# Kernel tuning notes

Hardware: AMD Instinct MI355X
Metric: run time of the kernel (lower is better)

Reference implementation:

```python
import jax, jax.numpy as jnp
import numpy as np

EMB = 1024
HEADS = 16
HEAD_DIM = EMB // HEADS


def setup_inputs() -> dict:
    key = jax.random.key(0)
    ks = jax.random.split(key, 9)
    s = 1.0 / np.sqrt(EMB)
    x = jax.random.normal(ks[0], (4, 2048, EMB), dtype=jnp.float32)
    Wq = jax.random.uniform(ks[1], (EMB, EMB), minval=-s, maxval=s, dtype=jnp.float32)
    bq = jax.random.uniform(ks[2], (EMB,), minval=-s, maxval=s, dtype=jnp.float32)
    Wk = jax.random.uniform(ks[3], (EMB, EMB), minval=-s, maxval=s, dtype=jnp.float32)
    bk = jax.random.uniform(ks[4], (EMB,), minval=-s, maxval=s, dtype=jnp.float32)
    Wv = jax.random.uniform(ks[5], (EMB, EMB), minval=-s, maxval=s, dtype=jnp.float32)
    bv = jax.random.uniform(ks[6], (EMB,), minval=-s, maxval=s, dtype=jnp.float32)
    Wo = jax.random.uniform(ks[7], (EMB, EMB), minval=-s, maxval=s, dtype=jnp.float32)
    bo = jax.random.uniform(ks[8], (EMB,), minval=-s, maxval=s, dtype=jnp.float32)
    return {"x": x, "Wq": Wq, "bq": bq, "Wk": Wk, "bk": bk, "Wv": Wv, "bv": bv, "Wo": Wo, "bo": bo}


def reference(x, Wq, bq, Wk, bk, Wv, bv, Wo, bo):
    B, S, E = x.shape
    # QKV projections (torch Linear: y = x W^T + b)
    q = x @ Wq.T + bq
    k = x @ Wk.T + bk
    v = x @ Wv.T + bv
    # split heads -> [B, H, S, Dh]
    q = q.reshape(B, S, HEADS, HEAD_DIM).transpose(0, 2, 1, 3)
    k = k.reshape(B, S, HEADS, HEAD_DIM).transpose(0, 2, 1, 3)
    v = v.reshape(B, S, HEADS, HEAD_DIM).transpose(0, 2, 1, 3)
    # NOTE: module scales by 1/sqrt(emb_size), NOT 1/sqrt(head_dim)
    scale = 1.0 / jnp.sqrt(jnp.asarray(E, dtype=x.dtype))
    energy = jnp.einsum('bhqd,bhkd->bhqk', q, k) * scale
    attention = jax.nn.softmax(energy, axis=-1)
    out = jnp.einsum('bhqk,bhkd->bhqd', attention, v)
    out = out.transpose(0, 2, 1, 3).reshape(B, S, E)
    return out @ Wo.T + bo
```

## Files before the change

kernel.cpp:

```cpp
#include <hip/hip_runtime.h>


typedef __bf16 bf16;
typedef __attribute__((ext_vector_type(8))) short short8;
typedef __attribute__((ext_vector_type(4))) float floatx4;
typedef __attribute__((ext_vector_type(2))) unsigned int uintx2;
typedef __attribute__((ext_vector_type(4))) unsigned int uintx4;

#define MFMA16(a, b, c) __builtin_amdgcn_mfma_f32_16x16x32_bf16((a), (b), (c), 0, 0, 0)

#define LDS_STRIDE 56

__device__ __forceinline__ float fast_exp2(float x) {
    float r;
    asm("v_exp_f32 %0, %1" : "=v"(r) : "v"(x));
    return r;
}
__device__ __forceinline__ unsigned int cvt_pk_bf16(float lo, float hi) {
    unsigned int r;
    asm("v_cvt_pk_bf16_f32 %0, %1, %2" : "=v"(r) : "v"(lo), "v"(hi));
    return r;
}

__device__ __forceinline__ void async16(const bf16* __restrict__ g, short* l) {
    __builtin_amdgcn_global_load_lds((const __attribute__((address_space(1))) void*)g,
                                     (__attribute__((address_space(3))) void*)l, 16, 0, 0);
}

__device__ __forceinline__ short8 frag8(const bf16* __restrict__ p) {
    return *(const short8*)p;
}
__device__ __forceinline__ short8 frag8(const float* __restrict__ p) {
    const floatx4 a = *(const floatx4*)p;
    const floatx4 b = *(const floatx4*)(p + 4);
    short8 r;
#pragma unroll
    for (int j = 0; j < 4; j++) {
        r[j]     = __builtin_bit_cast(short, (bf16)a[j]);
        r[4 + j] = __builtin_bit_cast(short, (bf16)b[j]);
    }
    return r;
}

__global__ __launch_bounds__(256) void to_bf16(
    const float* __restrict__ in, bf16* __restrict__ out, int n8)
{
    const int i = blockIdx.x * 256 + threadIdx.x;
    if (i >= n8) return;
    const floatx4 a = *(const floatx4*)(in + (size_t)i * 8);
    const floatx4 b = *(const floatx4*)(in + (size_t)i * 8 + 4);
    short8 r;
#pragma unroll
    for (int j = 0; j < 4; j++) {
        r[j]     = __builtin_bit_cast(short, (bf16)a[j]);
        r[4 + j] = __builtin_bit_cast(short, (bf16)b[j]);
    }
    *(short8*)((short*)out + (size_t)i * 8) = r;
}

template <typename TB>
__device__ __forceinline__ void gemm128_async(
    const bf16* __restrict__ A, const TB* __restrict__ B,
    int m0, int n0, short* As, short* Bs, floatx4 acc[4][4])
{
    constexpr bool BASYNC = (sizeof(TB) == 2);
    const int tid  = threadIdx.x;
    const int lane = tid & 63;
    const int w    = tid >> 6;
    const int wu   = __builtin_amdgcn_readfirstlane(w);
    const int wm   = w >> 1, wn = w & 1;
    const int g    = lane >> 4, c = lane & 15;
    const int ar = lane >> 2;
    const int aq = ((lane & 3) ^ (ar & 3)) * 8;
    const int lrow = tid >> 2;
    const int lc8  = (tid & 3) * 8;

#pragma unroll
    for (int mi = 0; mi < 4; mi++)
#pragma unroll
        for (int ni = 0; ni < 4; ni++)
            acc[mi][ni] = (floatx4){0.f, 0.f, 0.f, 0.f};

    const int aswz = (g ^ (c & 3)) * 8;

    for (int k0 = 0; k0 < 1024; k0 += 32) {
        async16(A + (size_t)(m0 + w * 32 + ar) * 1024 + k0 + aq,      As + wu * 1024);
        async16(A + (size_t)(m0 + w * 32 + 16 + ar) * 1024 + k0 + aq, As + wu * 1024 + 512);
        if constexpr (BASYNC) {
            const bf16* Bb = (const bf16*)B;
            async16(Bb + (size_t)(n0 + w * 32 + ar) * 1024 + k0 + aq,      Bs + wu * 1024);
            async16(Bb + (size_t)(n0 + w * 32 + 16 + ar) * 1024 + k0 + aq, Bs + wu * 1024 + 512);
        } else {
            *(short8*)(Bs + lrow * LDS_STRIDE + lc8) =
                frag8(B + (size_t)(n0 + lrow) * 1024 + k0 + lc8);
            *(short8*)(Bs + (lrow + 64) * LDS_STRIDE + lc8) =
                frag8(B + (size_t)(n0 + lrow + 64) * 1024 + k0 + lc8);
        }
        __syncthreads();

        short8 af[4], bfr[4];
#pragma unroll
        for (int mi = 0; mi < 4; mi++)
            af[mi] = *(const short8*)(As + (wm * 64 + mi * 16 + c) * 32 + aswz);
#pragma unroll
        for (int ni = 0; ni < 4; ni++) {
            if constexpr (BASYNC)
                bfr[ni] = *(const short8*)(Bs + (wn * 64 + ni * 16 + c) * 32 + aswz);
            else
                bfr[ni] = *(const short8*)(Bs + (wn * 64 + ni * 16 + c) * LDS_STRIDE + g * 8);
        }
#pragma unroll
        for (int mi = 0; mi < 4; mi++)
#pragma unroll
            for (int ni = 0; ni < 4; ni++)
                acc[mi][ni] = MFMA16(af[mi], bfr[ni], acc[mi][ni]);
        __syncthreads();
    }
}

template <typename TB>
__global__ __launch_bounds__(256) void qkv_gemm(
    const bf16* __restrict__ Xb,
    const TB* __restrict__ Wq, const TB* __restrict__ Wk, const TB* __restrict__ Wv,
    const float* __restrict__ bq, const float* __restrict__ bk, const float* __restrict__ bv,
    bf16* __restrict__ qkv)
{
    __shared__ __align__(16) short As[128 * 32];
    __shared__ __align__(16) short Bs[(sizeof(TB) == 2) ? 128 * 32 : 128 * LDS_STRIDE];

    const int z = blockIdx.z;
    const TB* W       = (z == 0) ? Wq : (z == 1) ? Wk : Wv;
    const float* bias = (z == 0) ? bq : (z == 1) ? bk : bv;
    bf16* outz = qkv + (size_t)z * (8192u * 1024u);

    const int m0 = blockIdx.y * 128;
    const int n0 = blockIdx.x * 128;

    floatx4 acc[4][4];
    gemm128_async(Xb, W, m0, n0, As, Bs, acc);

    const int lane = threadIdx.x & 63;
    const int w = threadIdx.x >> 6;
    const int wm = w >> 1, wn = w & 1;
    const int g = lane >> 4, c = lane & 15;

#pragma unroll
    for (int ni = 0; ni < 4; ni++) {
        const int n = n0 + wn * 64 + ni * 16 + c;
        const float bb = bias[n];
        const int h = n >> 6, d = n & 63;
#pragma unroll
        for (int mi = 0; mi < 4; mi++) {
#pragma unroll
            for (int r = 0; r < 4; r++) {
                const int m = m0 + wm * 64 + mi * 16 + g * 4 + r;
                const int b = m >> 11, s = m & 2047;
                const size_t idx = (z == 2)
                    ? ((((size_t)((b << 4) | h)) * 64 + d) * 2048 + s)
                    : ((((size_t)((b << 4) | h)) * 2048 + s) * 64 + d);
                outz[idx] = (bf16)(acc[mi][ni][r] + bb);
            }
        }
    }
}

__global__ __launch_bounds__(256, 2) void attn_kernel(
    const bf16* __restrict__ qkv, bf16* __restrict__ attn_out)
{
    __shared__ __align__(16) short Ks[2][128 * 64];
    __shared__ __align__(16) short Vs[2][64 * 128];

    const int linear = blockIdx.y * gridDim.x + blockIdx.x;
    const int slot = linear >> 3;
    const int bh = (linear & 7) * 8 + (slot >> 4);
    const int q0 = (slot & 15) * 128;

    const size_t HSTRIDE = 2048u * 64u;
    const bf16* __restrict__ Q  = qkv + (size_t)bh * HSTRIDE;
    const bf16* __restrict__ Kp = qkv + 8192u * 1024u + (size_t)bh * HSTRIDE;
    const bf16* __restrict__ Vt = qkv + 2u * 8192u * 1024u + (size_t)bh * HSTRIDE;

    const int tid  = threadIdx.x;
    const int lane = tid & 63;
    const int w    = tid >> 6;
    const int wu   = __builtin_amdgcn_readfirstlane(w);
    const int g    = lane >> 4, c = lane & 15;

    const float C2 = 0.04508422002778f;

    const int krow_off = lane >> 3;
    const int kchunk   = (lane & 7) ^ (lane >> 3);
    const int vrow_off = lane >> 4;

    short8 qf[2][2];
#pragma unroll
    for (int qb = 0; qb < 2; qb++)
#pragma unroll
        for (int ks = 0; ks < 2; ks++)
            qf[qb][ks] = *(const short8*)(Q + (size_t)(q0 + w * 32 + qb * 16 + c) * 64
                                            + ks * 32 + g * 8);

    floatx4 o[2][4];
#pragma unroll
    for (int mi = 0; mi < 2; mi++)
#pragma unroll
        for (int di = 0; di < 4; di++)
            o[mi][di] = (floatx4){0.f, 0.f, 0.f, 0.f};
    float m_run[2] = {-1e30f, -1e30f};
    float l_run[2] = {0.f, 0.f};

#pragma unroll
    for (int s = 0; s < 4; s++) {
        const int row = w * 32 + s * 8 + krow_off;
        async16(Kp + (size_t)row * 64 + kchunk * 8, &Ks[0][(wu * 32 + s * 8) * 64]);
    }
#pragma unroll
    for (int s = 0; s < 4; s++) {
        const int row = w * 16 + s * 4 + vrow_off;
        const int vchunk = (lane & 15) ^ (row & 15);
        async16(Vt + (size_t)row * 2048 + vchunk * 8, &Vs[0][(wu * 16 + s * 4) * 128]);
    }
    __syncthreads();

    int cur = 0;
    for (int kb = 0; kb < 16; kb++) {
        if (kb < 15) {
            const int kn = (kb + 1) * 128;
#pragma unroll
            for (int s = 0; s < 4; s++) {
                const int row = w * 32 + s * 8 + krow_off;
                async16(Kp + (size_t)(kn + row) * 64 + kchunk * 8,
                        &Ks[cur ^ 1][(wu * 32 + s * 8) * 64]);
            }
#pragma unroll
            for (int s = 0; s < 4; s++) {
                const int row = w * 16 + s * 4 + vrow_off;
                const int vchunk = (lane & 15) ^ (row & 15);
                async16(Vt + (size_t)row * 2048 + kn + vchunk * 8,
                        &Vs[cur ^ 1][(wu * 16 + s * 4) * 128]);
            }
        }

        const short* __restrict__ Kc = &Ks[cur][0];
        const short* __restrict__ Vc = &Vs[cur][0];

        floatx4 sAcc[2][8];
#pragma unroll
        for (int qb = 0; qb < 2; qb++)
#pragma unroll
            for (int ni = 0; ni < 8; ni++)
                sAcc[qb][ni] = (floatx4){0.f, 0.f, 0.f, 0.f};
#pragma unroll
        for (int ks = 0; ks < 2; ks++)
#pragma unroll
            for (int ni = 0; ni < 8; ni++) {
                const short8 kf = *(const short8*)(
                    Kc + (16 * ni + c) * 64 + (((ks * 4 + g) ^ (c & 7)) * 8));
                sAcc[0][ni] = MFMA16(kf, qf[0][ks], sAcc[0][ni]);
                sAcc[1][ni] = MFMA16(kf, qf[1][ks], sAcc[1][ni]);
            }

        float alpha[2];
        unsigned int lo[2][8], hi[2][8];
#pragma unroll
        for (int qb = 0; qb < 2; qb++) {
            floatx4 mv = sAcc[qb][0];
#pragma unroll
            for (int ni = 1; ni < 8; ni++)
#pragma unroll
                for (int r = 0; r < 4; r++) mv[r] = fmaxf(mv[r], sAcc[qb][ni][r]);
            float mx = fmaxf(fmaxf(mv[0], mv[1]), fmaxf(mv[2], mv[3]));
            mx = fmaxf(mx, __shfl_xor(mx, 16));
            mx = fmaxf(mx, __shfl_xor(mx, 32));
            const float mnew = fmaxf(m_run[qb], mx * C2);
            alpha[qb] = fast_exp2(m_run[qb] - mnew);
            m_run[qb] = mnew;

            floatx4 sv = {0.f, 0.f, 0.f, 0.f};
#pragma unroll
            for (int ni = 0; ni < 8; ni++) {
#pragma unroll
                for (int r = 0; r < 4; r++) {
                    const float p = fast_exp2(fmaf(sAcc[qb][ni][r], C2, -mnew));
                    sAcc[qb][ni][r] = p;
                    sv[r] += p;
                }
                lo[qb][ni] = cvt_pk_bf16(sAcc[qb][ni][0], sAcc[qb][ni][1]);
                hi[qb][ni] = cvt_pk_bf16(sAcc[qb][ni][2], sAcc[qb][ni][3]);
            }
            float sum = (sv[0] + sv[1]) + (sv[2] + sv[3]);
            sum += __shfl_xor(sum, 16);
            sum += __shfl_xor(sum, 32);
            l_run[qb] = l_run[qb] * alpha[qb] + sum;
        }

#pragma unroll
        for (int mi = 0; mi < 2; mi++)
#pragma unroll
            for (int r = 0; r < 4; r++) {
                const int src = (lane & 48) | (g * 4 + r);
                const float a = __shfl(alpha[mi], src);
#pragma unroll
                for (int di = 0; di < 4; di++) o[mi][di][r] *= a;
            }

#pragma unroll
        for (int t = 0; t < 4; t++) {
            const short8 pf0 = __builtin_bit_cast(short8,
                (uintx4){lo[0][2 * t], hi[0][2 * t], lo[0][2 * t + 1], hi[0][2 * t + 1]});
            const short8 pf1 = __builtin_bit_cast(short8,
                (uintx4){lo[1][2 * t], hi[1][2 * t], lo[1][2 * t + 1], hi[1][2 * t + 1]});
#pragma unroll
            for (int di = 0; di < 4; di++) {
                const int rowb = (16 * di + c) * 128 + 4 * (g & 1);
                const uintx2 vlo = *(const uintx2*)(
                    Vc + rowb + (((4 * t + (g >> 1)) ^ c) * 8));
                const uintx2 vhi = *(const uintx2*)(
                    Vc + rowb + (((4 * t + 2 + (g >> 1)) ^ c) * 8));
                const short8 vf = __builtin_bit_cast(short8,
                    (uintx4){vlo[0], vlo[1], vhi[0], vhi[1]});
                o[0][di] = MFMA16(pf0, vf, o[0][di]);
                o[1][di] = MFMA16(pf1, vf, o[1][di]);
            }
        }

        if (kb < 15) __syncthreads();
        cur ^= 1;
    }

    const int b = bh >> 4, h = bh & 15;
#pragma unroll
    for (int mi = 0; mi < 2; mi++) {
#pragma unroll
        for (int r = 0; r < 4; r++) {
            const int src = (lane & 48) | (g * 4 + r);
            const float linv = 1.0f / __shfl(l_run[mi], src);
            const int srow = q0 + w * 32 + mi * 16 + g * 4 + r;
#pragma unroll
            for (int di = 0; di < 4; di++) {
                attn_out[((size_t)(b * 2048 + srow)) * 1024 + h * 64 + di * 16 + c] =
                    (bf16)(o[mi][di][r] * linv);
            }
        }
    }
}

template <typename TB>
__global__ __launch_bounds__(256) void out_gemm(
    const bf16* __restrict__ A, const TB* __restrict__ Wo,
    const float* __restrict__ bo, float* __restrict__ C)
{
    __shared__ __align__(16) short As[128 * 32];
    __shared__ __align__(16) short Bs[(sizeof(TB) == 2) ? 128 * 32 : 128 * LDS_STRIDE];

    const int m0 = blockIdx.y * 128;
    const int n0 = blockIdx.x * 128;

    floatx4 acc[4][4];
    gemm128_async(A, Wo, m0, n0, As, Bs, acc);

    const int lane = threadIdx.x & 63;
    const int w = threadIdx.x >> 6;
    const int wm = w >> 1, wn = w & 1;
    const int g = lane >> 4, c = lane & 15;

#pragma unroll
    for (int ni = 0; ni < 4; ni++) {
        const int n = n0 + wn * 64 + ni * 16 + c;
        const float bb = bo[n];
#pragma unroll
        for (int mi = 0; mi < 4; mi++) {
#pragma unroll
            for (int r = 0; r < 4; r++) {
                const int m = m0 + wm * 64 + mi * 16 + g * 4 + r;
                C[(size_t)m * 1024 + n] = acc[mi][ni][r] + bb;
            }
        }
    }
}

extern "C" void kernel_launch(void* const* d_in, const int* in_sizes, int n_in,
                              void* d_out, int out_size, void* d_ws, size_t ws_size,
                              hipStream_t stream)
{
    const float* x  = (const float*)d_in[0];
    const float* Wq = (const float*)d_in[1];
    const float* bq = (const float*)d_in[2];
    const float* Wk = (const float*)d_in[3];
    const float* bk = (const float*)d_in[4];
    const float* Wv = (const float*)d_in[5];
    const float* bv = (const float*)d_in[6];
    const float* Wo = (const float*)d_in[7];
    const float* bo = (const float*)d_in[8];
    float* out = (float*)d_out;

    bf16* qkv  = (bf16*)d_ws;
    bf16* attn = qkv + 3u * 8192u * 1024u;
    bf16* xb   = attn;

    const size_t base = 64u * 1024u * 1024u;
    const bool haveW = ws_size >= base + 8u * 1024u * 1024u;
    bf16* wb = (bf16*)((char*)d_ws + base);

    to_bf16<<<dim3(4096), dim3(256), 0, stream>>>(x, xb, 1048576);

    if (haveW) {
        to_bf16<<<dim3(512), dim3(256), 0, stream>>>(Wq, wb + 0u * 1048576u, 131072);
        to_bf16<<<dim3(512), dim3(256), 0, stream>>>(Wk, wb + 1u * 1048576u, 131072);
        to_bf16<<<dim3(512), dim3(256), 0, stream>>>(Wv, wb + 2u * 1048576u, 131072);
        to_bf16<<<dim3(512), dim3(256), 0, stream>>>(Wo, wb + 3u * 1048576u, 131072);
        qkv_gemm<bf16><<<dim3(8, 64, 3), dim3(256), 0, stream>>>(
            xb, wb, wb + 1048576u, wb + 2u * 1048576u, bq, bk, bv, qkv);
    } else {
        qkv_gemm<float><<<dim3(8, 64, 3), dim3(256), 0, stream>>>(
            xb, Wq, Wk, Wv, bq, bk, bv, qkv);
    }

    attn_kernel<<<dim3(16, 64), dim3(256), 0, stream>>>(qkv, attn);

    if (haveW) {
        out_gemm<bf16><<<dim3(8, 64), dim3(256), 0, stream>>>(
            attn, wb + 3u * 1048576u, bo, out);
    } else {
        out_gemm<float><<<dim3(8, 64), dim3(256), 0, stream>>>(attn, Wo, bo, out);
    }
}
```

Before: 339.7 us.

## Double-buffer LDS in bf16 GEMMs, fuse weight casts, vectorize V-transpose stores

Adds a double-buffered GEMM main loop for the bf16 weight path: the async loads for the next K tile are issued before computing on the current tile, with one barrier per iteration instead of two. This is meant to hide global-to-LDS latency behind the MFMA work. The four weight-cast launches are merged into one kernel, and the transposed V epilogue now writes four contiguous bf16 values with a single vector store. LDS use per block doubles, which may lower occupancy.

```diff
diff --git a/kernel.cpp b/kernel.cpp
--- a/kernel.cpp
+++ b/kernel.cpp
@@ -2,6 +2,7 @@
 
 
 typedef __bf16 bf16;
+typedef __attribute__((ext_vector_type(4))) short shortx4;
 typedef __attribute__((ext_vector_type(8))) short short8;
 typedef __attribute__((ext_vector_type(4))) float floatx4;
 typedef __attribute__((ext_vector_type(2))) unsigned int uintx2;
@@ -58,12 +59,93 @@
     *(short8*)((short*)out + (size_t)i * 8) = r;
 }
 
-template <typename TB>
-__device__ __forceinline__ void gemm128_async(
-    const bf16* __restrict__ A, const TB* __restrict__ B,
+__global__ __launch_bounds__(256) void to_bf16_w4(
+    const float* __restrict__ Wq, const float* __restrict__ Wk,
+    const float* __restrict__ Wv, const float* __restrict__ Wo,
+    bf16* __restrict__ out)
+{
+    const int i = blockIdx.x * 256 + threadIdx.x;
+    const int t = i >> 17;
+    const int j = i & 131071;
+    const float* src = (t == 0) ? Wq : (t == 1) ? Wk : (t == 2) ? Wv : Wo;
+    const floatx4 a = *(const floatx4*)(src + (size_t)j * 8);
+    const floatx4 b = *(const floatx4*)(src + (size_t)j * 8 + 4);
+    short8 r;
+#pragma unroll
+    for (int jj = 0; jj < 4; jj++) {
+        r[jj]     = __builtin_bit_cast(short, (bf16)a[jj]);
+        r[4 + jj] = __builtin_bit_cast(short, (bf16)b[jj]);
+    }
+    *(short8*)((short*)out + (size_t)t * 1048576 + (size_t)j * 8) = r;
+}
+
+__device__ __forceinline__ void gemm128_db(
+    const bf16* __restrict__ A, const bf16* __restrict__ B,
     int m0, int n0, short* As, short* Bs, floatx4 acc[4][4])
 {
-    constexpr bool BASYNC = (sizeof(TB) == 2);
+    const int tid  = threadIdx.x;
+    const int lane = tid & 63;
+    const int w    = tid >> 6;
+    const int wu   = __builtin_amdgcn_readfirstlane(w);
+    const int wm   = w >> 1, wn = w & 1;
+    const int g    = lane >> 4, c = lane & 15;
+    const int ar   = lane >> 2;
+    const int aq   = ((lane & 3) ^ (ar & 3)) * 8;
+    const int aswz = (g ^ (c & 3)) * 8;
+
+#pragma unroll
+    for (int mi = 0; mi < 4; mi++)
+#pragma unroll
+        for (int ni = 0; ni < 4; ni++)
+            acc[mi][ni] = (floatx4){0.f, 0.f, 0.f, 0.f};
+
+    const bf16* Arow0 = A + (size_t)(m0 + w * 32 + ar) * 1024 + aq;
+    const bf16* Arow1 = A + (size_t)(m0 + w * 32 + 16 + ar) * 1024 + aq;
+    const bf16* Brow0 = B + (size_t)(n0 + w * 32 + ar) * 1024 + aq;
+    const bf16* Brow1 = B + (size_t)(n0 + w * 32 + 16 + ar) * 1024 + aq;
+
+    async16(Arow0, As + wu * 1024);
+    async16(Arow1, As + wu * 1024 + 512);
+    async16(Brow0, Bs + wu * 1024);
+    async16(Brow1, Bs + wu * 1024 + 512);
+    __syncthreads();
+
+    int cur = 0;
+    for (int k0 = 0; k0 < 1024; k0 += 32) {
+        if (k0 < 992) {
+            const int kn = k0 + 32;
+            short* Ad = As + (cur ^ 1) * 4096 + wu * 1024;
+            short* Bd = Bs + (cur ^ 1) * 4096 + wu * 1024;
+            async16(Arow0 + kn, Ad);
+            async16(Arow1 + kn, Ad + 512);
+            async16(Brow0 + kn, Bd);
+            async16(Brow1 + kn, Bd + 512);
+        }
+
+        const short* Ac = As + cur * 4096;
+        const short* Bc = Bs + cur * 4096;
+        short8 af[4], bfr[4];
+#pragma unroll
+        for (int mi = 0; mi < 4; mi++)
+            af[mi] = *(const short8*)(Ac + (wm * 64 + mi * 16 + c) * 32 + aswz);
+#pragma unroll
+        for (int ni = 0; ni < 4; ni++)
+            bfr[ni] = *(const short8*)(Bc + (wn * 64 + ni * 16 + c) * 32 + aswz);
+#pragma unroll
+        for (int mi = 0; mi < 4; mi++)
+#pragma unroll
+            for (int ni = 0; ni < 4; ni++)
+                acc[mi][ni] = MFMA16(af[mi], bfr[ni], acc[mi][ni]);
+
+        if (k0 < 992) __syncthreads();
+        cur ^= 1;
+    }
+}
+
+__device__ __forceinline__ void gemm128_fallback(
+    const bf16* __restrict__ A, const float* __restrict__ B,
+    int m0, int n0, short* As, short* Bs, floatx4 acc[4][4])
+{
     const int tid  = threadIdx.x;
     const int lane = tid & 63;
     const int w    = tid >> 6;
@@ -86,16 +168,10 @@
     for (int k0 = 0; k0 < 1024; k0 += 32) {
         async16(A + (size_t)(m0 + w * 32 + ar) * 1024 + k0 + aq,      As + wu * 1024);
         async16(A + (size_t)(m0 + w * 32 + 16 + ar) * 1024 + k0 + aq, As + wu * 1024 + 512);
-        if constexpr (BASYNC) {
-            const bf16* Bb = (const bf16*)B;
-            async16(Bb + (size_t)(n0 + w * 32 + ar) * 1024 + k0 + aq,      Bs + wu * 1024);
-            async16(Bb + (size_t)(n0 + w * 32 + 16 + ar) * 1024 + k0 + aq, Bs + wu * 1024 + 512);
-        } else {
-            *(short8*)(Bs + lrow * LDS_STRIDE + lc8) =
-                frag8(B + (size_t)(n0 + lrow) * 1024 + k0 + lc8);
-            *(short8*)(Bs + (lrow + 64) * LDS_STRIDE + lc8) =
-                frag8(B + (size_t)(n0 + lrow + 64) * 1024 + k0 + lc8);
-        }
+        *(short8*)(Bs + lrow * LDS_STRIDE + lc8) =
+            frag8(B + (size_t)(n0 + lrow) * 1024 + k0 + lc8);
+        *(short8*)(Bs + (lrow + 64) * LDS_STRIDE + lc8) =
+            frag8(B + (size_t)(n0 + lrow + 64) * 1024 + k0 + lc8);
         __syncthreads();
 
         short8 af[4], bfr[4];
@@ -103,12 +179,8 @@
         for (int mi = 0; mi < 4; mi++)
             af[mi] = *(const short8*)(As + (wm * 64 + mi * 16 + c) * 32 + aswz);
 #pragma unroll
-        for (int ni = 0; ni < 4; ni++) {
-            if constexpr (BASYNC)
-                bfr[ni] = *(const short8*)(Bs + (wn * 64 + ni * 16 + c) * 32 + aswz);
-            else
-                bfr[ni] = *(const short8*)(Bs + (wn * 64 + ni * 16 + c) * LDS_STRIDE + g * 8);
-        }
+        for (int ni = 0; ni < 4; ni++)
+            bfr[ni] = *(const short8*)(Bs + (wn * 64 + ni * 16 + c) * LDS_STRIDE + g * 8);
 #pragma unroll
         for (int mi = 0; mi < 4; mi++)
 #pragma unroll
@@ -125,8 +197,8 @@
     const float* __restrict__ bq, const float* __restrict__ bk, const float* __restrict__ bv,
     bf16* __restrict__ qkv)
 {
-    __shared__ __align__(16) short As[128 * 32];
-    __shared__ __align__(16) short Bs[(sizeof(TB) == 2) ? 128 * 32 : 128 * LDS_STRIDE];
+    __shared__ __align__(16) short As[(sizeof(TB) == 2) ? 8192 : 4096];
+    __shared__ __align__(16) short Bs[(sizeof(TB) == 2) ? 8192 : 128 * LDS_STRIDE];
 
     const int z = blockIdx.z;
     const TB* W       = (z == 0) ? Wq : (z == 1) ? Wk : Wv;
@@ -137,28 +209,48 @@
     const int n0 = blockIdx.x * 128;
 
     floatx4 acc[4][4];
-    gemm128_async(Xb, W, m0, n0, As, Bs, acc);
+    if constexpr (sizeof(TB) == 2)
+        gemm128_db(Xb, (const bf16*)W, m0, n0, As, Bs, acc);
+    else
+        gemm128_fallback(Xb, (const float*)W, m0, n0, As, Bs, acc);
 
     const int lane = threadIdx.x & 63;
     const int w = threadIdx.x >> 6;
     const int wm = w >> 1, wn = w & 1;
     const int g = lane >> 4, c = lane & 15;
 
-#pragma unroll
-    for (int ni = 0; ni < 4; ni++) {
-        const int n = n0 + wn * 64 + ni * 16 + c;
-        const float bb = bias[n];
-        const int h = n >> 6, d = n & 63;
-#pragma unroll
-        for (int mi = 0; mi < 4; mi++) {
-#pragma unroll
-            for (int r = 0; r < 4; r++) {
-                const int m = m0 + wm * 64 + mi * 16 + g * 4 + r;
+    if (z == 2) {
+#pragma unroll
+        for (int ni = 0; ni < 4; ni++) {
+            const int n = n0 + wn * 64 + ni * 16 + c;
+            const float bb = bias[n];
+            const int h = n >> 6, d = n & 63;
+#pragma unroll
+            for (int mi = 0; mi < 4; mi++) {
+                const int m = m0 + wm * 64 + mi * 16 + g * 4;
                 const int b = m >> 11, s = m & 2047;
-                const size_t idx = (z == 2)
-                    ? ((((size_t)((b << 4) | h)) * 64 + d) * 2048 + s)
-                    : ((((size_t)((b << 4) | h)) * 2048 + s) * 64 + d);
-                outz[idx] = (bf16)(acc[mi][ni][r] + bb);
+                shortx4 st;
+#pragma unroll
+                for (int r = 0; r < 4; r++)
+                    st[r] = __builtin_bit_cast(short, (bf16)(acc[mi][ni][r] + bb));
+                *(shortx4*)&outz[(((size_t)((b << 4) | h)) * 64 + d) * 2048 + s] = st;
+            }
+        }
+    } else {
+#pragma unroll
+        for (int ni = 0; ni < 4; ni++) {
+            const int n = n0 + wn * 64 + ni * 16 + c;
+            const float bb = bias[n];
+            const int h = n >> 6, d = n & 63;
+#pragma unroll
+            for (int mi = 0; mi < 4; mi++) {
+#pragma unroll
+                for (int r = 0; r < 4; r++) {
+                    const int m = m0 + wm * 64 + mi * 16 + g * 4 + r;
+                    const int b = m >> 11, s = m & 2047;
+                    outz[(((size_t)((b << 4) | h)) * 2048 + s) * 64 + d] =
+                        (bf16)(acc[mi][ni][r] + bb);
+                }
             }
         }
     }
@@ -350,14 +442,17 @@
     const bf16* __restrict__ A, const TB* __restrict__ Wo,
     const float* __restrict__ bo, float* __restrict__ C)
 {
-    __shared__ __align__(16) short As[128 * 32];
-    __shared__ __align__(16) short Bs[(sizeof(TB) == 2) ? 128 * 32 : 128 * LDS_STRIDE];
+    __shared__ __align__(16) short As[(sizeof(TB) == 2) ? 8192 : 4096];
+    __shared__ __align__(16) short Bs[(sizeof(TB) == 2) ? 8192 : 128 * LDS_STRIDE];
 
     const int m0 = blockIdx.y * 128;
     const int n0 = blockIdx.x * 128;
 
     floatx4 acc[4][4];
-    gemm128_async(A, Wo, m0, n0, As, Bs, acc);
+    if constexpr (sizeof(TB) == 2)
+        gemm128_db(A, (const bf16*)Wo, m0, n0, As, Bs, acc);
+    else
+        gemm128_fallback(A, (const float*)Wo, m0, n0, As, Bs, acc);
 
     const int lane = threadIdx.x & 63;
     const int w = threadIdx.x >> 6;
@@ -405,10 +500,7 @@
     to_bf16<<<dim3(4096), dim3(256), 0, stream>>>(x, xb, 1048576);
 
     if (haveW) {
-        to_bf16<<<dim3(512), dim3(256), 0, stream>>>(Wq, wb + 0u * 1048576u, 131072);
-        to_bf16<<<dim3(512), dim3(256), 0, stream>>>(Wk, wb + 1u * 1048576u, 131072);
-        to_bf16<<<dim3(512), dim3(256), 0, stream>>>(Wv, wb + 2u * 1048576u, 131072);
-        to_bf16<<<dim3(512), dim3(256), 0, stream>>>(Wo, wb + 3u * 1048576u, 131072);
+        to_bf16_w4<<<dim3(2048), dim3(256), 0, stream>>>(Wq, Wk, Wv, Wo, wb);
         qkv_gemm<bf16><<<dim3(8, 64, 3), dim3(256), 0, stream>>>(
             xb, wb, wb + 1048576u, wb + 2u * 1048576u, bq, bk, bv, qkv);
     } else {
```

Measured after the change: 343.1 us. About the same (+1.0%).
